# Performance work log

Measured on AMD Instinct MI355X. Metric: run time of the kernel, lower is better.

The kernel has to match this reference:

```python
import jax, jax.numpy as jnp
import numpy as np

NEG_SLOPE = 0.2  # PyG GATConv default leaky_relu slope
BN_EPS = 1e-5


def gat_conv(x, src, dst, num_nodes, W, a_src, a_dst, bias, concat):
    """PyG-style GATConv (eval mode, self-loops already appended to src/dst)."""
    H, F = a_src.shape
    h = (x @ W).reshape(num_nodes, H, F)              # [N,H,F]
    e_src = jnp.einsum('nhf,hf->nh', h, a_src)        # [N,H]
    e_dst = jnp.einsum('nhf,hf->nh', h, a_dst)        # [N,H]
    e = jax.nn.leaky_relu(e_src[src] + e_dst[dst], NEG_SLOPE)  # [E,H]
    m = jax.ops.segment_max(e, dst, num_segments=num_nodes)    # segment softmax (stable)
    w = jnp.exp(e - m[dst])
    z = jax.ops.segment_sum(w, dst, num_segments=num_nodes)
    alpha = w / (z[dst] + 1e-16)                      # [E,H]
    msg = alpha[:, :, None] * h[src]                  # [E,H,F]
    out = jax.ops.segment_sum(msg, dst, num_segments=num_nodes)  # [N,H,F]
    out = out.reshape(num_nodes, H * F) if concat else out.mean(axis=1)
    return out + bias


def bn_eval(x, gamma, beta):
    # BatchNorm1d eval with initialized running stats (mean=0, var=1)
    return x * (gamma / jnp.sqrt(1.0 + BN_EPS)) + beta


def setup_inputs() -> dict:
    key = jax.random.key(0)
    ks = jax.random.split(key, 16)
    N, E, Fin, H, Fh, MLP = 50000, 800000, 128, 4, 32, 64
    HF = H * Fh  # 128
    s = 0.05
    inp = {
        'x': jax.random.normal(ks[0], (N, Fin), jnp.float32),
        'edge_index': jax.random.randint(ks[1], (2, E), 0, N, jnp.int64),
        # conv0: Fin -> Fh per head, concat
        'W1': jax.random.normal(ks[2], (Fin, HF), jnp.float32) * s,
        'a1s': jax.random.normal(ks[3], (H, Fh), jnp.float32) * s,
        'a1d': jax.random.normal(ks[4], (H, Fh), jnp.float32) * s,
        'b1': jnp.zeros((HF,), jnp.float32),
        # conv1: HF -> Fh per head, concat
        'W2': jax.random.normal(ks[5], (HF, HF), jnp.float32) * s,
        'a2s': jax.random.normal(ks[6], (H, Fh), jnp.float32) * s,
        'a2d': jax.random.normal(ks[7], (H, Fh), jnp.float32) * s,
        'b2': jnp.zeros((HF,), jnp.float32),
        # mlp block 0
        'M1w': jax.random.normal(ks[8], (HF, MLP), jnp.float32) * s,
        'M1b': jnp.zeros((MLP,), jnp.float32),
        'g1': jnp.ones((MLP,), jnp.float32),
        'be1': jnp.zeros((MLP,), jnp.float32),
        'M2w': jax.random.normal(ks[9], (MLP, HF), jnp.float32) * s,
        'M2b': jnp.zeros((HF,), jnp.float32),
        'g2': jnp.ones((HF,), jnp.float32),
        'be2': jnp.zeros((HF,), jnp.float32),
        # conv2: HF -> Fh per head, mean over heads (concat=False)
        'W3': jax.random.normal(ks[10], (HF, HF), jnp.float32) * s,
        'a3s': jax.random.normal(ks[11], (H, Fh), jnp.float32) * s,
        'a3d': jax.random.normal(ks[12], (H, Fh), jnp.float32) * s,
        'b3': jnp.zeros((Fh,), jnp.float32),
    }
    return inp


def reference(x, edge_index, W1, a1s, a1d, b1, W2, a2s, a2d, b2,
              M1w, M1b, g1, be1, M2w, M2b, g2, be2, W3, a3s, a3d, b3):
    N = x.shape[0]
    loops = jnp.arange(N, dtype=edge_index.dtype)
    src = jnp.concatenate([edge_index[0], loops])  # add self-loops (PyG default)
    dst = jnp.concatenate([edge_index[1], loops])

    # layer 0: conv -> relu -> (dropout=id, eval) -> mlp[0]
    h = jax.nn.relu(gat_conv(x, src, dst, N, W1, a1s, a1d, b1, concat=True))
    h = bn_eval(jax.nn.relu(h @ M1w + M1b), g1, be1)
    h = bn_eval(jax.nn.relu(h @ M2w + M2b), g2, be2)

    # layer 1: conv -> relu -> (dropout=id)
    h = jax.nn.relu(gat_conv(h, src, dst, N, W2, a2s, a2d, b2, concat=True))

    # output layer: concat=False -> mean over heads
    out = gat_conv(h, src, dst, N, W3, a3s, a3d, b3, concat=False)
    return out
```

## Files before the change

kernel.cpp:

```cpp
#include <hip/hip_runtime.h>
#include <hip/hip_bf16.h>

#define NEG_SLOPE 0.2f
#define BN_RS 0.9999950000374997f

typedef __attribute__((ext_vector_type(8))) _Float16 f16x8;
typedef __attribute__((ext_vector_type(2))) _Float16 f16x2;
typedef __attribute__((ext_vector_type(4))) float f32x4;

__device__ __forceinline__ void store_split(float w, _Float16* H, _Float16* L, size_t off) {
  _Float16 h = (_Float16)w;
  H[off] = h;
  L[off] = (_Float16)(w - (float)h);
}


__global__ void zero256(int* p) { p[threadIdx.x] = 0; }

__global__ void eb_hist(const int* __restrict__ ei, int* __restrict__ bucketSize, int E) {
  __shared__ int h[256];
  int tid = threadIdx.x;
  h[tid] = 0;
  __syncthreads();
  for (int i = blockIdx.x * 256 + tid; i < E; i += gridDim.x * 256)
    atomicAdd(&h[ei[E + i] >> 8], 1);
  __syncthreads();
  if (h[tid]) atomicAdd(&bucketSize[tid], h[tid]);
}

__global__ void eb_scan(const int* __restrict__ bucketSize, int* __restrict__ edgeStart,
                        int* __restrict__ cursor, int* __restrict__ csrStart, int N) {
  __shared__ int sd[256];
  int tid = threadIdx.x;
  int v = bucketSize[tid];
  sd[tid] = v;
  __syncthreads();
  for (int off = 1; off < 256; off <<= 1) {
    int t = (tid >= off) ? sd[tid - off] : 0;
    __syncthreads();
    sd[tid] += t;
    __syncthreads();
  }
  int excl = sd[tid] - v;
  edgeStart[tid] = excl;
  cursor[tid] = excl;
  csrStart[tid] = excl + min(tid << 8, N);
  if (tid == 255) edgeStart[256] = sd[255];
}

#define PCH 4096
__global__ __launch_bounds__(256) void eb_part(const int* __restrict__ ei,
                                               int* __restrict__ cursor,
                                               unsigned* __restrict__ staging, int E) {
  __shared__ unsigned val[PCH];
  __shared__ unsigned char bk[PCH];
  __shared__ int cnt[256];
  __shared__ int base[256];
  int tid = threadIdx.x;
  cnt[tid] = 0;
  __syncthreads();
  int e0 = blockIdx.x * PCH;
  int n = min(PCH, E - e0);
  for (int j = tid; j < n; j += 256) {
    int s = ei[e0 + j], d = ei[E + e0 + j];
    val[j] = ((unsigned)(d & 255) << 16) | (unsigned)s;
    int b = d >> 8;
    bk[j] = (unsigned char)b;
    atomicAdd(&cnt[b], 1);
  }
  __syncthreads();
  if (cnt[tid]) base[tid] = atomicAdd(&cursor[tid], cnt[tid]);
  __syncthreads();
  for (int j = tid; j < n; j += 256) {
    int b = bk[j];
    int off = atomicSub(&cnt[b], 1) - 1;
    staging[base[b] + off] = val[j];
  }
}

__global__ __launch_bounds__(256) void eb_csr(
    const unsigned* __restrict__ staging, const int* __restrict__ edgeStart,
    const int* __restrict__ csrStart, int* __restrict__ rowptr,
    int* __restrict__ csr, int N) {
  __shared__ int deg[256];
  __shared__ int sc[256];
  __shared__ int ex[256];
  int b = blockIdx.x, tid = threadIdx.x;
  int n0 = b << 8;
  int nn = min(256, N - n0);
  deg[tid] = (tid < nn) ? 1 : 0;
  __syncthreads();
  int s0 = edgeStart[b], s1 = edgeStart[b + 1];
  for (int j = s0 + tid; j < s1; j += 256)
    atomicAdd(&deg[staging[j] >> 16], 1);
  __syncthreads();
  int dv = deg[tid];
  sc[tid] = dv;
  __syncthreads();
  for (int off = 1; off < 256; off <<= 1) {
    int t = (tid >= off) ? sc[tid - off] : 0;
    __syncthreads();
    sc[tid] += t;
    __syncthreads();
  }
  int incl = sc[tid];
  int cbase = csrStart[b];
  ex[tid] = incl - dv;
  if (tid < nn) {
    rowptr[n0 + tid + 1] = cbase + incl;
    csr[cbase + incl - 1] = n0 + tid;
  }
  if (b == 0 && tid == 0) rowptr[0] = 0;
  deg[tid] = 0;
  __syncthreads();
  for (int j = s0 + tid; j < s1; j += 256) {
    unsigned v = staging[j];
    int dl = v >> 16;
    int src = v & 0xFFFF;
    int off = atomicAdd(&deg[dl], 1);
    csr[cbase + ex[dl] + off] = src;
  }
}

__device__ __forceinline__ void wprep_conv(const float* __restrict__ W,
                                           const float* __restrict__ as_,
                                           const float* __restrict__ ad_,
                                           _Float16* __restrict__ H, _Float16* __restrict__ L,
                                           int lb, int tid) {
  if (lb < 64) {
    int idx = lb * 256 + tid;
    int k = idx >> 7, p = idx & 127;
    store_split(W[k * 128 + p], H, L, (size_t)p * 128 + k);
  } else if (lb < 68) {
    int idx = (lb - 64) * 256 + tid;
    int rl = idx >> 7, k = idx & 127;
    const float* a = (rl < 4) ? as_ : ad_;
    int h = rl & 3;
    float s = 0.f;
#pragma unroll
    for (int f = 0; f < 32; f++) s += W[k * 128 + h * 32 + f] * a[h * 32 + f];
    store_split(s, H, L, (size_t)(128 + rl) * 128 + k);
  } else {
    int idx = (lb - 68) * 256 + tid;
    int rl = idx >> 7, k = idx & 127;
    H[(size_t)(136 + rl) * 128 + k] = (_Float16)0.f;
    L[(size_t)(136 + rl) * 128 + k] = (_Float16)0.f;
  }
}

__global__ void wprep_all(
    const float* __restrict__ W1, const float* __restrict__ a1s, const float* __restrict__ a1d,
    _Float16* __restrict__ W1H, _Float16* __restrict__ W1L,
    const float* __restrict__ W2, const float* __restrict__ a2s, const float* __restrict__ a2d,
    _Float16* __restrict__ W2H, _Float16* __restrict__ W2L,
    const float* __restrict__ W3, const float* __restrict__ a3s, const float* __restrict__ a3d,
    _Float16* __restrict__ W3H, _Float16* __restrict__ W3L,
    const float* __restrict__ M1, _Float16* __restrict__ M1H, _Float16* __restrict__ M1L,
    const float* __restrict__ M2, _Float16* __restrict__ M2H, _Float16* __restrict__ M2L) {
  int b = blockIdx.x, tid = threadIdx.x;
  if (b < 72)       wprep_conv(W1, a1s, a1d, W1H, W1L, b, tid);
  else if (b < 144) wprep_conv(W2, a2s, a2d, W2H, W2L, b - 72, tid);
  else if (b < 216) wprep_conv(W3, a3s, a3d, W3H, W3L, b - 144, tid);
  else if (b < 248) {
    int idx = (b - 216) * 256 + tid;
    int k = idx >> 6, p = idx & 63;
    store_split(M1[k * 64 + p], M1H, M1L, (size_t)p * 128 + k);
  } else {
    int idx = (b - 248) * 256 + tid;
    int k = idx >> 7, p = idx & 127;
    store_split(M2[k * 128 + p], M2H, M2L, (size_t)p * 64 + k);
  }
}

template <int PT, int PST, int K, int EPI, int AUG, typename TA>
__global__ __launch_bounds__(256) void gemm_f16(
    const TA* __restrict__ A, const _Float16* __restrict__ WtH,
    const _Float16* __restrict__ WtL, _Float16* __restrict__ C, int N,
    const float* __restrict__ bias, const float* __restrict__ gamma,
    const float* __restrict__ beta, float* __restrict__ esb,
    float* __restrict__ edb) {
  constexpr int NTILE = PT / 16;
  constexpr int CTB = NTILE / 4;
  constexpr int REM = NTILE % 4;
  constexpr int KT = K / 32;
  __shared__ _Float16 As[128 * 32];
  __shared__ _Float16 WsH[PT * 32];
  __shared__ _Float16 WsL[PT * 32];
  const int tid = threadIdx.x;
  const int wave = tid >> 6, lane = tid & 63;
  const int quad = lane >> 4, l16 = lane & 15;
  const int row0 = blockIdx.x * 128;
  const bool xw = (REM != 0) && (wave == 0);

  f32x4 acc[8][CTB + (REM ? 1 : 0)];
#pragma unroll
  for (int rt = 0; rt < 8; rt++)
#pragma unroll
    for (int nt = 0; nt < CTB + (REM ? 1 : 0); nt++) acc[rt][nt] = (f32x4){0.f, 0.f, 0.f, 0.f};

  for (int kc = 0; kc < KT; ++kc) {
    {
      int r = tid >> 1, part = tid & 1;
      int gr = row0 + r;
      _Float16* dst = &As[r * 32 + part * 16];
      if (gr < N) {
        const TA* src = A + (size_t)gr * K + kc * 32 + part * 16;
        if constexpr (sizeof(TA) == 4) {
          f16x8 h0, h1;
#pragma unroll
          for (int j = 0; j < 8; j++) { h0[j] = (_Float16)src[j]; h1[j] = (_Float16)src[8 + j]; }
          *(f16x8*)dst = h0; *(f16x8*)(dst + 8) = h1;
        } else {
          uint4 v0 = *(const uint4*)src;
          uint4 v1 = *(const uint4*)(src + 8);
          *(uint4*)dst = v0; *(uint4*)(dst + 8) = v1;
        }
      } else {
        *(uint4*)dst = make_uint4(0, 0, 0, 0);
        *(uint4*)(dst + 8) = make_uint4(0, 0, 0, 0);
      }
    }
    for (int idx = tid; idx < PT * 2; idx += 256) {
      int isL = idx >= PT;
      int p = isL ? idx - PT : idx;
      const _Float16* src = (isL ? WtL : WtH) + (size_t)p * K + kc * 32;
      _Float16* dst = (isL ? WsL : WsH) + p * 32;
      uint4 a0 = *(const uint4*)src;       uint4 a1 = *(const uint4*)(src + 8);
      uint4 a2 = *(const uint4*)(src + 16); uint4 a3 = *(const uint4*)(src + 24);
      *(uint4*)dst = a0; *(uint4*)(dst + 8) = a1;
      *(uint4*)(dst + 16) = a2; *(uint4*)(dst + 24) = a3;
    }
    __syncthreads();

    f16x8 bh[CTB], bl[CTB], bhE, blE;
#pragma unroll
    for (int nt = 0; nt < CTB; nt++) {
      int p = (wave * CTB + nt) * 16 + l16;
      bh[nt] = *(f16x8*)&WsH[p * 32 + quad * 8];
      bl[nt] = *(f16x8*)&WsL[p * 32 + quad * 8];
    }
    if constexpr (REM) {
      if (xw) {
        int p = 4 * CTB * 16 + l16;
        bhE = *(f16x8*)&WsH[p * 32 + quad * 8];
        blE = *(f16x8*)&WsL[p * 32 + quad * 8];
      }
    }
#pragma unroll
    for (int rt = 0; rt < 8; rt++) {
      f16x8 a = *(f16x8*)&As[(rt * 16 + l16) * 32 + quad * 8];
#pragma unroll
      for (int nt = 0; nt < CTB; nt++) {
        acc[rt][nt] = __builtin_amdgcn_mfma_f32_16x16x32_f16(a, bh[nt], acc[rt][nt], 0, 0, 0);
        acc[rt][nt] = __builtin_amdgcn_mfma_f32_16x16x32_f16(a, bl[nt], acc[rt][nt], 0, 0, 0);
      }
      if constexpr (REM) {
        if (xw) {
          acc[rt][CTB] = __builtin_amdgcn_mfma_f32_16x16x32_f16(a, bhE, acc[rt][CTB], 0, 0, 0);
          acc[rt][CTB] = __builtin_amdgcn_mfma_f32_16x16x32_f16(a, blE, acc[rt][CTB], 0, 0, 0);
        }
      }
    }
    __syncthreads();
  }

#pragma unroll
  for (int nt = 0; nt < CTB; nt++) {
    int c = (wave * CTB + nt) * 16 + l16;
    float bi = 0.f, ga = 0.f, be = 0.f;
    if constexpr (EPI == 1) { bi = bias[c]; ga = gamma[c] * BN_RS; be = beta[c]; }
#pragma unroll
    for (int rt = 0; rt < 8; rt++)
#pragma unroll
      for (int g = 0; g < 4; g++) {
        int r = row0 + rt * 16 + quad * 4 + g;
        if (r < N) {
          float v = acc[rt][nt][g];
          if constexpr (EPI == 1) { v += bi; v = v > 0.f ? v : 0.f; v = v * ga + be; }
          C[(size_t)r * PST + c] = (_Float16)v;
        }
      }
  }
  if constexpr (REM) {
    if (wave == 0 && l16 < 8) {
      float* dstb = (l16 < 4) ? esb : edb;
      int h = l16 & 3;
#pragma unroll
      for (int rt = 0; rt < 8; rt++)
#pragma unroll
        for (int g = 0; g < 4; g++) {
          int r = row0 + rt * 16 + quad * 4 + g;
          if (r < N) dstb[(size_t)r * 4 + h] = acc[rt][CTB][g];
        }
    }
  }
}

template <int MODE>
__global__ __launch_bounds__(256) void gat_agg(
    const _Float16* __restrict__ hx, const int* __restrict__ rowptr,
    const int* __restrict__ csr, const float* __restrict__ es,
    const float* __restrict__ ed, const float* __restrict__ bias,
    void* __restrict__ outp, int N) {
  __shared__ float wbuf[4][16][4];
  int wid = (blockIdx.x * 256 + threadIdx.x) >> 6;
  if (wid >= N) return;
  int wave = threadIdx.x >> 6;
  int lane = threadIdx.x & 63;
  int head = lane >> 4;
  int j4 = lane >> 2;
  int h4 = lane & 3;
  int beg = rowptr[wid], end = rowptr[wid + 1];
  float edv4 = ed[wid * 4 + h4];
  float ax = 0.f, ay = 0.f, z = 0.f;
  const _Float16* hb = hx + 2 * lane;

  for (int c = beg; c < end; c += 16) {
    int m = end - c; if (m > 16) m = 16;
    if (j4 < m) {
      int s = csr[c + j4];
      float t = es[s * 4 + h4] + edv4;
      t = t > 0.f ? t : NEG_SLOPE * t;
      wbuf[wave][j4][h4] = __expf(t);
    }
    int j = 0;
    for (; j + 4 <= m; j += 4) {
      int e = c + j;
      int s0 = csr[e], s1 = csr[e + 1], s2 = csr[e + 2], s3 = csr[e + 3];
      float w0 = wbuf[wave][j + 0][head];
      float w1 = wbuf[wave][j + 1][head];
      float w2 = wbuf[wave][j + 2][head];
      float w3 = wbuf[wave][j + 3][head];
      f16x2 h0 = *(const f16x2*)(hb + (size_t)s0 * 128);
      f16x2 h1 = *(const f16x2*)(hb + (size_t)s1 * 128);
      f16x2 h2 = *(const f16x2*)(hb + (size_t)s2 * 128);
      f16x2 h3 = *(const f16x2*)(hb + (size_t)s3 * 128);
      z += (w0 + w1) + (w2 + w3);
      ax = fmaf(w0, (float)h0[0], ax); ay = fmaf(w0, (float)h0[1], ay);
      ax = fmaf(w1, (float)h1[0], ax); ay = fmaf(w1, (float)h1[1], ay);
      ax = fmaf(w2, (float)h2[0], ax); ay = fmaf(w2, (float)h2[1], ay);
      ax = fmaf(w3, (float)h3[0], ax); ay = fmaf(w3, (float)h3[1], ay);
    }
    for (; j < m; ++j) {
      int s = csr[c + j];
      float w = wbuf[wave][j][head];
      f16x2 hv = *(const f16x2*)(hb + (size_t)s * 128);
      z += w;
      ax = fmaf(w, (float)hv[0], ax);
      ay = fmaf(w, (float)hv[1], ay);
    }
  }
  float inv = 1.f / (z + 1e-16f);
  float vx = ax * inv, vy = ay * inv;
  if (MODE == 0) {
    vx += bias[2 * lane]; vy += bias[2 * lane + 1];
    vx = vx > 0.f ? vx : 0.f;  vy = vy > 0.f ? vy : 0.f;
    f16x2 o; o[0] = (_Float16)vx; o[1] = (_Float16)vy;
    *(f16x2*)((_Float16*)outp + (size_t)wid * 128 + 2 * lane) = o;
  } else {
    vx += __shfl_xor(vx, 16); vx += __shfl_xor(vx, 32);
    vy += __shfl_xor(vy, 16); vy += __shfl_xor(vy, 32);
    if (lane < 16) {
      float ox = vx * 0.25f + bias[2 * lane];
      float oy = vy * 0.25f + bias[2 * lane + 1];
      *(float2*)((float*)outp + (size_t)wid * 32 + 2 * lane) = make_float2(ox, oy);
    }
  }
}

extern "C" void kernel_launch(void* const* d_in, const int* in_sizes, int n_in,
                              void* d_out, int out_size, void* d_ws, size_t ws_size,
                              hipStream_t stream) {
  const float* x   = (const float*)d_in[0];
  const int*   ei  = (const int*)d_in[1];
  const float* W1  = (const float*)d_in[2];
  const float* a1s = (const float*)d_in[3];
  const float* a1d = (const float*)d_in[4];
  const float* b1  = (const float*)d_in[5];
  const float* W2  = (const float*)d_in[6];
  const float* a2s = (const float*)d_in[7];
  const float* a2d = (const float*)d_in[8];
  const float* b2  = (const float*)d_in[9];
  const float* M1w = (const float*)d_in[10];
  const float* M1b = (const float*)d_in[11];
  const float* g1  = (const float*)d_in[12];
  const float* be1 = (const float*)d_in[13];
  const float* M2w = (const float*)d_in[14];
  const float* M2b = (const float*)d_in[15];
  const float* g2  = (const float*)d_in[16];
  const float* be2 = (const float*)d_in[17];
  const float* W3  = (const float*)d_in[18];
  const float* a3s = (const float*)d_in[19];
  const float* a3d = (const float*)d_in[20];
  const float* b3  = (const float*)d_in[21];

  const int N = in_sizes[0] / 128;
  const int E = in_sizes[1] / 2;

  char* w = (char*)d_ws;
  _Float16* bufA = (_Float16*)w; w += (size_t)N * 128 * 2;
  _Float16* bufB = (_Float16*)w; w += (size_t)N * 128 * 2;
  _Float16* bufM = (_Float16*)w; w += (size_t)N * 64 * 2;
  float* esb  = (float*)w; w += (size_t)N * 4 * 4;
  float* edb  = (float*)w; w += (size_t)N * 4 * 4;
  int* rowptr = (int*)w;   w += (size_t)(N + 1) * 4;
  int* csr    = (int*)w;   w += (size_t)(E + N) * 4;
  unsigned* staging = (unsigned*)w; w += (size_t)E * 4;
  int* bucketSize = (int*)w; w += 256 * 4;
  int* edgeStart  = (int*)w; w += 257 * 4;
  int* cursor     = (int*)w; w += 256 * 4;
  int* csrStart   = (int*)w; w += 256 * 4;
  _Float16* W1H = (_Float16*)w; w += 144 * 128 * 2;
  _Float16* W1L = (_Float16*)w; w += 144 * 128 * 2;
  _Float16* W2H = (_Float16*)w; w += 144 * 128 * 2;
  _Float16* W2L = (_Float16*)w; w += 144 * 128 * 2;
  _Float16* W3H = (_Float16*)w; w += 144 * 128 * 2;
  _Float16* W3L = (_Float16*)w; w += 144 * 128 * 2;
  _Float16* M1H = (_Float16*)w; w += 64 * 128 * 2;
  _Float16* M1L = (_Float16*)w; w += 64 * 128 * 2;
  _Float16* M2H = (_Float16*)w; w += 128 * 64 * 2;
  _Float16* M2L = (_Float16*)w; w += 128 * 64 * 2;

  const int gb = (N + 127) / 128;
  const int aggb = (N + 3) / 4;
  const int nbk = (N + 255) / 256;
  const int pbk = (E + PCH - 1) / PCH;

  wprep_all<<<280, 256, 0, stream>>>(W1, a1s, a1d, W1H, W1L,
                                     W2, a2s, a2d, W2H, W2L,
                                     W3, a3s, a3d, W3H, W3L,
                                     M1w, M1H, M1L, M2w, M2H, M2L);

  zero256<<<1, 256, 0, stream>>>(bucketSize);
  eb_hist<<<256, 256, 0, stream>>>(ei, bucketSize, E);
  eb_scan<<<1, 256, 0, stream>>>(bucketSize, edgeStart, cursor, csrStart, N);
  eb_part<<<pbk, 256, 0, stream>>>(ei, cursor, staging, E);
  eb_csr<<<nbk, 256, 0, stream>>>(staging, edgeStart, csrStart, rowptr, csr, N);

  gemm_f16<144, 128, 128, 0, 1, float><<<gb, 256, 0, stream>>>(
      x, W1H, W1L, bufA, N, nullptr, nullptr, nullptr, esb, edb);
  gat_agg<0><<<aggb, 256, 0, stream>>>(bufA, rowptr, csr, esb, edb, b1, bufB, N);
  gemm_f16<64, 64, 128, 1, 0, _Float16><<<gb, 256, 0, stream>>>(
      bufB, M1H, M1L, bufM, N, M1b, g1, be1, nullptr, nullptr);
  gemm_f16<128, 128, 64, 1, 0, _Float16><<<gb, 256, 0, stream>>>(
      bufM, M2H, M2L, bufA, N, M2b, g2, be2, nullptr, nullptr);

  gemm_f16<144, 128, 128, 0, 1, _Float16><<<gb, 256, 0, stream>>>(
      bufA, W2H, W2L, bufB, N, nullptr, nullptr, nullptr, esb, edb);
  gat_agg<0><<<aggb, 256, 0, stream>>>(bufB, rowptr, csr, esb, edb, b2, bufA, N);

  gemm_f16<144, 128, 128, 0, 1, _Float16><<<gb, 256, 0, stream>>>(
      bufA, W3H, W3L, bufB, N, nullptr, nullptr, nullptr, esb, edb);
  gat_agg<1><<<aggb, 256, 0, stream>>>(bufB, rowptr, csr, esb, edb, b3, d_out, N);
}
```

Before: 373.2 us.

## Fuse MLP GEMMs and software-pipeline GAT aggregation with staged source indices

```diff
diff --git a/kernel.cpp b/kernel.cpp
--- a/kernel.cpp
+++ b/kernel.cpp
@@ -81,7 +81,7 @@
 __global__ __launch_bounds__(256) void eb_csr(
     const unsigned* __restrict__ staging, const int* __restrict__ edgeStart,
     const int* __restrict__ csrStart, int* __restrict__ rowptr,
-    int* __restrict__ csr, int N) {
+    unsigned* __restrict__ csr, int N) {
   __shared__ int deg[256];
   __shared__ int sc[256];
   __shared__ int ex[256];
@@ -108,7 +108,8 @@
   ex[tid] = incl - dv;
   if (tid < nn) {
     rowptr[n0 + tid + 1] = cbase + incl;
-    csr[cbase + incl - 1] = n0 + tid;
+    unsigned me = (unsigned)(n0 + tid);
+    csr[cbase + incl - 1] = (me << 16) | me;
   }
   if (b == 0 && tid == 0) rowptr[0] = 0;
   deg[tid] = 0;
@@ -116,9 +117,9 @@
   for (int j = s0 + tid; j < s1; j += 256) {
     unsigned v = staging[j];
     int dl = v >> 16;
-    int src = v & 0xFFFF;
+    unsigned src = v & 0xFFFF;
     int off = atomicAdd(&deg[dl], 1);
-    csr[cbase + ex[dl] + off] = src;
+    csr[cbase + ex[dl] + off] = ((unsigned)(n0 + dl) << 16) | src;
   }
 }
 
@@ -172,16 +173,13 @@
   }
 }
 
-template <int PT, int PST, int K, int EPI, int AUG, typename TA>
+template <typename TA>
 __global__ __launch_bounds__(256) void gemm_f16(
     const TA* __restrict__ A, const _Float16* __restrict__ WtH,
     const _Float16* __restrict__ WtL, _Float16* __restrict__ C, int N,
-    const float* __restrict__ bias, const float* __restrict__ gamma,
-    const float* __restrict__ beta, float* __restrict__ esb,
-    float* __restrict__ edb) {
-  constexpr int NTILE = PT / 16;
-  constexpr int CTB = NTILE / 4;
-  constexpr int REM = NTILE % 4;
+    float* __restrict__ esb, float* __restrict__ edb) {
+  constexpr int PT = 144, PST = 128, K = 128;
+  constexpr int CTB = 2;
   constexpr int KT = K / 32;
   __shared__ _Float16 As[128 * 32];
   __shared__ _Float16 WsH[PT * 32];
@@ -190,13 +188,13 @@
   const int wave = tid >> 6, lane = tid & 63;
   const int quad = lane >> 4, l16 = lane & 15;
   const int row0 = blockIdx.x * 128;
-  const bool xw = (REM != 0) && (wave == 0);
-
-  f32x4 acc[8][CTB + (REM ? 1 : 0)];
+  const bool xw = (wave == 0);
+
+  f32x4 acc[8][CTB + 1];
 #pragma unroll
   for (int rt = 0; rt < 8; rt++)
 #pragma unroll
-    for (int nt = 0; nt < CTB + (REM ? 1 : 0); nt++) acc[rt][nt] = (f32x4){0.f, 0.f, 0.f, 0.f};
+    for (int nt = 0; nt < CTB + 1; nt++) acc[rt][nt] = (f32x4){0.f, 0.f, 0.f, 0.f};
 
   for (int kc = 0; kc < KT; ++kc) {
     {
@@ -239,12 +237,10 @@
       bh[nt] = *(f16x8*)&WsH[p * 32 + quad * 8];
       bl[nt] = *(f16x8*)&WsL[p * 32 + quad * 8];
     }
-    if constexpr (REM) {
-      if (xw) {
-        int p = 4 * CTB * 16 + l16;
-        bhE = *(f16x8*)&WsH[p * 32 + quad * 8];
-        blE = *(f16x8*)&WsL[p * 32 + quad * 8];
-      }
+    if (xw) {
+      int p = 4 * CTB * 16 + l16;
+      bhE = *(f16x8*)&WsH[p * 32 + quad * 8];
+      blE = *(f16x8*)&WsL[p * 32 + quad * 8];
     }
 #pragma unroll
     for (int rt = 0; rt < 8; rt++) {
@@ -254,11 +250,9 @@
         acc[rt][nt] = __builtin_amdgcn_mfma_f32_16x16x32_f16(a, bh[nt], acc[rt][nt], 0, 0, 0);
         acc[rt][nt] = __builtin_amdgcn_mfma_f32_16x16x32_f16(a, bl[nt], acc[rt][nt], 0, 0, 0);
       }
-      if constexpr (REM) {
-        if (xw) {
-          acc[rt][CTB] = __builtin_amdgcn_mfma_f32_16x16x32_f16(a, bhE, acc[rt][CTB], 0, 0, 0);
-          acc[rt][CTB] = __builtin_amdgcn_mfma_f32_16x16x32_f16(a, blE, acc[rt][CTB], 0, 0, 0);
-        }
+      if (xw) {
+        acc[rt][CTB] = __builtin_amdgcn_mfma_f32_16x16x32_f16(a, bhE, acc[rt][CTB], 0, 0, 0);
+        acc[rt][CTB] = __builtin_amdgcn_mfma_f32_16x16x32_f16(a, blE, acc[rt][CTB], 0, 0, 0);
       }
     }
     __syncthreads();
@@ -267,88 +261,235 @@
 #pragma unroll
   for (int nt = 0; nt < CTB; nt++) {
     int c = (wave * CTB + nt) * 16 + l16;
-    float bi = 0.f, ga = 0.f, be = 0.f;
-    if constexpr (EPI == 1) { bi = bias[c]; ga = gamma[c] * BN_RS; be = beta[c]; }
+#pragma unroll
+    for (int rt = 0; rt < 8; rt++)
+#pragma unroll
+      for (int g = 0; g < 4; g++) {
+        int r = row0 + rt * 16 + quad * 4 + g;
+        if (r < N) C[(size_t)r * PST + c] = (_Float16)acc[rt][nt][g];
+      }
+  }
+  if (wave == 0 && l16 < 8) {
+    float* dstb = (l16 < 4) ? esb : edb;
+    int h = l16 & 3;
+#pragma unroll
+    for (int rt = 0; rt < 8; rt++)
+#pragma unroll
+      for (int g = 0; g < 4; g++) {
+        int r = row0 + rt * 16 + quad * 4 + g;
+        if (r < N) dstb[(size_t)r * 4 + h] = acc[rt][CTB][g];
+      }
+  }
+}
+
+__global__ __launch_bounds__(256) void mlp_fused(
+    const _Float16* __restrict__ A,
+    const _Float16* __restrict__ M1H, const _Float16* __restrict__ M1L,
+    const _Float16* __restrict__ M2H, const _Float16* __restrict__ M2L,
+    _Float16* __restrict__ C, int N,
+    const float* __restrict__ b1v, const float* __restrict__ g1v, const float* __restrict__ be1v,
+    const float* __restrict__ b2v, const float* __restrict__ g2v, const float* __restrict__ be2v) {
+  __shared__ _Float16 As[128 * 32];
+  __shared__ _Float16 W1Hs[64 * 32], W1Ls[64 * 32];
+  __shared__ _Float16 T[128 * 72];
+  __shared__ _Float16 W2Hs[128 * 32], W2Ls[128 * 32];
+  const int tid = threadIdx.x;
+  const int wave = tid >> 6, lane = tid & 63;
+  const int quad = lane >> 4, l16 = lane & 15;
+  const int row0 = blockIdx.x * 128;
+
+  f32x4 acc1[8];
+#pragma unroll
+  for (int rt = 0; rt < 8; rt++) acc1[rt] = (f32x4){0.f, 0.f, 0.f, 0.f};
+  for (int kc = 0; kc < 4; ++kc) {
+    {
+      int r = tid >> 1, part = tid & 1;
+      int gr = row0 + r;
+      _Float16* dst = &As[r * 32 + part * 16];
+      if (gr < N) {
+        const _Float16* src = A + (size_t)gr * 128 + kc * 32 + part * 16;
+        uint4 v0 = *(const uint4*)src;
+        uint4 v1 = *(const uint4*)(src + 8);
+        *(uint4*)dst = v0; *(uint4*)(dst + 8) = v1;
+      } else {
+        *(uint4*)dst = make_uint4(0, 0, 0, 0);
+        *(uint4*)(dst + 8) = make_uint4(0, 0, 0, 0);
+      }
+    }
+    if (tid < 128) {
+      int isL = tid >= 64;
+      int p = tid & 63;
+      const _Float16* src = (isL ? M1L : M1H) + (size_t)p * 128 + kc * 32;
+      _Float16* dst = (isL ? W1Ls : W1Hs) + p * 32;
+      uint4 a0 = *(const uint4*)src;       uint4 a1 = *(const uint4*)(src + 8);
+      uint4 a2 = *(const uint4*)(src + 16); uint4 a3 = *(const uint4*)(src + 24);
+      *(uint4*)dst = a0; *(uint4*)(dst + 8) = a1;
+      *(uint4*)(dst + 16) = a2; *(uint4*)(dst + 24) = a3;
+    }
+    __syncthreads();
+    int p = wave * 16 + l16;
+    f16x8 bh = *(f16x8*)&W1Hs[p * 32 + quad * 8];
+    f16x8 bl = *(f16x8*)&W1Ls[p * 32 + quad * 8];
+#pragma unroll
+    for (int rt = 0; rt < 8; rt++) {
+      f16x8 a = *(f16x8*)&As[(rt * 16 + l16) * 32 + quad * 8];
+      acc1[rt] = __builtin_amdgcn_mfma_f32_16x16x32_f16(a, bh, acc1[rt], 0, 0, 0);
+      acc1[rt] = __builtin_amdgcn_mfma_f32_16x16x32_f16(a, bl, acc1[rt], 0, 0, 0);
+    }
+    __syncthreads();
+  }
+  {
+    int c = wave * 16 + l16;
+    float bi = b1v[c], ga = g1v[c] * BN_RS, be = be1v[c];
+#pragma unroll
+    for (int rt = 0; rt < 8; rt++)
+#pragma unroll
+      for (int g = 0; g < 4; g++) {
+        int r = rt * 16 + quad * 4 + g;
+        float v = acc1[rt][g] + bi;
+        v = v > 0.f ? v : 0.f;
+        v = v * ga + be;
+        T[r * 72 + c] = (_Float16)v;
+      }
+  }
+  __syncthreads();
+
+  f32x4 acc2[8][2];
+#pragma unroll
+  for (int rt = 0; rt < 8; rt++)
+#pragma unroll
+    for (int nt = 0; nt < 2; nt++) acc2[rt][nt] = (f32x4){0.f, 0.f, 0.f, 0.f};
+  for (int kc = 0; kc < 2; ++kc) {
+    {
+      int isL = tid >= 128;
+      int p = tid & 127;
+      const _Float16* src = (isL ? M2L : M2H) + (size_t)p * 64 + kc * 32;
+      _Float16* dst = (isL ? W2Ls : W2Hs) + p * 32;
+      uint4 a0 = *(const uint4*)src;       uint4 a1 = *(const uint4*)(src + 8);
+      uint4 a2 = *(const uint4*)(src + 16); uint4 a3 = *(const uint4*)(src + 24);
+      *(uint4*)dst = a0; *(uint4*)(dst + 8) = a1;
+      *(uint4*)(dst + 16) = a2; *(uint4*)(dst + 24) = a3;
+    }
+    __syncthreads();
+    f16x8 bh[2], bl[2];
+#pragma unroll
+    for (int nt = 0; nt < 2; nt++) {
+      int p = (wave * 2 + nt) * 16 + l16;
+      bh[nt] = *(f16x8*)&W2Hs[p * 32 + quad * 8];
+      bl[nt] = *(f16x8*)&W2Ls[p * 32 + quad * 8];
+    }
+#pragma unroll
+    for (int rt = 0; rt < 8; rt++) {
+      f16x8 a = *(f16x8*)&T[(rt * 16 + l16) * 72 + kc * 32 + quad * 8];
+#pragma unroll
+      for (int nt = 0; nt < 2; nt++) {
+        acc2[rt][nt] = __builtin_amdgcn_mfma_f32_16x16x32_f16(a, bh[nt], acc2[rt][nt], 0, 0, 0);
+        acc2[rt][nt] = __builtin_amdgcn_mfma_f32_16x16x32_f16(a, bl[nt], acc2[rt][nt], 0, 0, 0);
+      }
+    }
+    __syncthreads();
+  }
+#pragma unroll
+  for (int nt = 0; nt < 2; nt++) {
+    int c = (wave * 2 + nt) * 16 + l16;
+    float bi = b2v[c], ga = g2v[c] * BN_RS, be = be2v[c];
 #pragma unroll
     for (int rt = 0; rt < 8; rt++)
 #pragma unroll
       for (int g = 0; g < 4; g++) {
         int r = row0 + rt * 16 + quad * 4 + g;
         if (r < N) {
-          float v = acc[rt][nt][g];
-          if constexpr (EPI == 1) { v += bi; v = v > 0.f ? v : 0.f; v = v * ga + be; }
-          C[(size_t)r * PST + c] = (_Float16)v;
+          float v = acc2[rt][nt][g] + bi;
+          v = v > 0.f ? v : 0.f;
+          v = v * ga + be;
+          C[(size_t)r * 128 + c] = (_Float16)v;
         }
       }
-  }
-  if constexpr (REM) {
-    if (wave == 0 && l16 < 8) {
-      float* dstb = (l16 < 4) ? esb : edb;
-      int h = l16 & 3;
-#pragma unroll
-      for (int rt = 0; rt < 8; rt++)
-#pragma unroll
-        for (int g = 0; g < 4; g++) {
-          int r = row0 + rt * 16 + quad * 4 + g;
-          if (r < N) dstb[(size_t)r * 4 + h] = acc[rt][CTB][g];
-        }
-    }
   }
 }
 
 template <int MODE>
 __global__ __launch_bounds__(256) void gat_agg(
     const _Float16* __restrict__ hx, const int* __restrict__ rowptr,
-    const int* __restrict__ csr, const float* __restrict__ es,
+    const unsigned* __restrict__ csr, const float* __restrict__ es,
     const float* __restrict__ ed, const float* __restrict__ bias,
     void* __restrict__ outp, int N) {
-  __shared__ float wbuf[4][16][4];
-  int wid = (blockIdx.x * 256 + threadIdx.x) >> 6;
+  __shared__ float wbuf[4][2][16][4];
+  __shared__ int sbuf[4][2][16];
+  int wid = __builtin_amdgcn_readfirstlane((int)((blockIdx.x * 256 + threadIdx.x) >> 6));
   if (wid >= N) return;
   int wave = threadIdx.x >> 6;
   int lane = threadIdx.x & 63;
   int head = lane >> 4;
-  int j4 = lane >> 2;
-  int h4 = lane & 3;
+  int j4 = lane >> 2, h4 = lane & 3;
   int beg = rowptr[wid], end = rowptr[wid + 1];
   float edv4 = ed[wid * 4 + h4];
   float ax = 0.f, ay = 0.f, z = 0.f;
   const _Float16* hb = hx + 2 * lane;
-
-  for (int c = beg; c < end; c += 16) {
-    int m = end - c; if (m > 16) m = 16;
+  int nch = (end - beg + 15) >> 4;
+
+  {
+    int m = end - beg; if (m > 16) m = 16;
     if (j4 < m) {
-      int s = csr[c + j4];
+      int s = (int)(csr[beg + j4] & 0xFFFFu);
       float t = es[s * 4 + h4] + edv4;
       t = t > 0.f ? t : NEG_SLOPE * t;
-      wbuf[wave][j4][h4] = __expf(t);
+      wbuf[wave][0][j4][h4] = __expf(t);
+      if (h4 == 0) sbuf[wave][0][j4] = s;
+    }
+  }
+  int pb = 0;
+  for (int ci = 0; ci < nch; ++ci) {
+    int c = beg + (ci << 4);
+    int m = end - c; if (m > 16) m = 16;
+    if (ci + 1 < nch) {
+      int c2 = c + 16;
+      int m2 = end - c2; if (m2 > 16) m2 = 16;
+      if (j4 < m2) {
+        int s = (int)(csr[c2 + j4] & 0xFFFFu);
+        float t = es[s * 4 + h4] + edv4;
+        t = t > 0.f ? t : NEG_SLOPE * t;
+        wbuf[wave][pb ^ 1][j4][h4] = __expf(t);
+        if (h4 == 0) sbuf[wave][pb ^ 1][j4] = s;
+      }
     }
     int j = 0;
-    for (; j + 4 <= m; j += 4) {
-      int e = c + j;
-      int s0 = csr[e], s1 = csr[e + 1], s2 = csr[e + 2], s3 = csr[e + 3];
-      float w0 = wbuf[wave][j + 0][head];
-      float w1 = wbuf[wave][j + 1][head];
-      float w2 = wbuf[wave][j + 2][head];
-      float w3 = wbuf[wave][j + 3][head];
+    for (; j + 8 <= m; j += 8) {
+      int s0 = sbuf[wave][pb][j + 0], s1 = sbuf[wave][pb][j + 1];
+      int s2 = sbuf[wave][pb][j + 2], s3 = sbuf[wave][pb][j + 3];
+      int s4 = sbuf[wave][pb][j + 4], s5 = sbuf[wave][pb][j + 5];
+      int s6 = sbuf[wave][pb][j + 6], s7 = sbuf[wave][pb][j + 7];
+      float w0 = wbuf[wave][pb][j + 0][head], w1 = wbuf[wave][pb][j + 1][head];
+      float w2 = wbuf[wave][pb][j + 2][head], w3 = wbuf[wave][pb][j + 3][head];
+      float w4 = wbuf[wave][pb][j + 4][head], w5 = wbuf[wave][pb][j + 5][head];
+      float w6 = wbuf[wave][pb][j + 6][head], w7 = wbuf[wave][pb][j + 7][head];
       f16x2 h0 = *(const f16x2*)(hb + (size_t)s0 * 128);
       f16x2 h1 = *(const f16x2*)(hb + (size_t)s1 * 128);
       f16x2 h2 = *(const f16x2*)(hb + (size_t)s2 * 128);
       f16x2 h3 = *(const f16x2*)(hb + (size_t)s3 * 128);
-      z += (w0 + w1) + (w2 + w3);
+      f16x2 h4v = *(const f16x2*)(hb + (size_t)s4 * 128);
+      f16x2 h5 = *(const f16x2*)(hb + (size_t)s5 * 128);
+      f16x2 h6 = *(const f16x2*)(hb + (size_t)s6 * 128);
+      f16x2 h7 = *(const f16x2*)(hb + (size_t)s7 * 128);
+      z += ((w0 + w1) + (w2 + w3)) + ((w4 + w5) + (w6 + w7));
       ax = fmaf(w0, (float)h0[0], ax); ay = fmaf(w0, (float)h0[1], ay);
       ax = fmaf(w1, (float)h1[0], ax); ay = fmaf(w1, (float)h1[1], ay);
       ax = fmaf(w2, (float)h2[0], ax); ay = fmaf(w2, (float)h2[1], ay);
       ax = fmaf(w3, (float)h3[0], ax); ay = fmaf(w3, (float)h3[1], ay);
+      ax = fmaf(w4, (float)h4v[0], ax); ay = fmaf(w4, (float)h4v[1], ay);
+      ax = fmaf(w5, (float)h5[0], ax); ay = fmaf(w5, (float)h5[1], ay);
+      ax = fmaf(w6, (float)h6[0], ax); ay = fmaf(w6, (float)h6[1], ay);
+      ax = fmaf(w7, (float)h7[0], ax); ay = fmaf(w7, (float)h7[1], ay);
     }
     for (; j < m; ++j) {
-      int s = csr[c + j];
-      float w = wbuf[wave][j][head];
+      int s = sbuf[wave][pb][j];
+      float w = wbuf[wave][pb][j][head];
       f16x2 hv = *(const f16x2*)(hb + (size_t)s * 128);
       z += w;
       ax = fmaf(w, (float)hv[0], ax);
       ay = fmaf(w, (float)hv[1], ay);
     }
+    pb ^= 1;
   }
   float inv = 1.f / (z + 1e-16f);
   float vx = ax * inv, vy = ay * inv;
@@ -396,15 +537,15 @@
 
   const int N = in_sizes[0] / 128;
   const int E = in_sizes[1] / 2;
+  const int S = E + N;
 
   char* w = (char*)d_ws;
   _Float16* bufA = (_Float16*)w; w += (size_t)N * 128 * 2;
   _Float16* bufB = (_Float16*)w; w += (size_t)N * 128 * 2;
-  _Float16* bufM = (_Float16*)w; w += (size_t)N * 64 * 2;
   float* esb  = (float*)w; w += (size_t)N * 4 * 4;
   float* edb  = (float*)w; w += (size_t)N * 4 * 4;
   int* rowptr = (int*)w;   w += (size_t)(N + 1) * 4;
-  int* csr    = (int*)w;   w += (size_t)(E + N) * 4;
+  unsigned* csr = (unsigned*)w; w += (size_t)S * 4;
   unsigned* staging = (unsigned*)w; w += (size_t)E * 4;
   int* bucketSize = (int*)w; w += 256 * 4;
   int* edgeStart  = (int*)w; w += 257 * 4;
@@ -437,19 +578,14 @@
   eb_part<<<pbk, 256, 0, stream>>>(ei, cursor, staging, E);
   eb_csr<<<nbk, 256, 0, stream>>>(staging, edgeStart, csrStart, rowptr, csr, N);
 
-  gemm_f16<144, 128, 128, 0, 1, float><<<gb, 256, 0, stream>>>(
-      x, W1H, W1L, bufA, N, nullptr, nullptr, nullptr, esb, edb);
+  gemm_f16<float><<<gb, 256, 0, stream>>>(x, W1H, W1L, bufA, N, esb, edb);
   gat_agg<0><<<aggb, 256, 0, stream>>>(bufA, rowptr, csr, esb, edb, b1, bufB, N);
-  gemm_f16<64, 64, 128, 1, 0, _Float16><<<gb, 256, 0, stream>>>(
-      bufB, M1H, M1L, bufM, N, M1b, g1, be1, nullptr, nullptr);
-  gemm_f16<128, 128, 64, 1, 0, _Float16><<<gb, 256, 0, stream>>>(
-      bufM, M2H, M2L, bufA, N, M2b, g2, be2, nullptr, nullptr);
-
-  gemm_f16<144, 128, 128, 0, 1, _Float16><<<gb, 256, 0, stream>>>(
-      bufA, W2H, W2L, bufB, N, nullptr, nullptr, nullptr, esb, edb);
+  mlp_fused<<<gb, 256, 0, stream>>>(bufB, M1H, M1L, M2H, M2L, bufA, N,
+                                    M1b, g1, be1, M2b, g2, be2);
+
+  gemm_f16<_Float16><<<gb, 256, 0, stream>>>(bufA, W2H, W2L, bufB, N, esb, edb);
   gat_agg<0><<<aggb, 256, 0, stream>>>(bufB, rowptr, csr, esb, edb, b2, bufA, N);
 
-  gemm_f16<144, 128, 128, 0, 1, _Float16><<<gb, 256, 0, stream>>>(
-      bufA, W3H, W3L, bufB, N, nullptr, nullptr, nullptr, esb, edb);
+  gemm_f16<_Float16><<<gb, 256, 0, stream>>>(bufA, W3H, W3L, bufB, N, esb, edb);
   gat_agg<1><<<aggb, 256, 0, stream>>>(bufB, rowptr, csr, esb, edb, b3, d_out, N);
 }
```

Result: faster. 336.8 us (-9.8%).
